# Performance work log

Hardware: AMD Instinct MI355X
Metric: run time of the kernel (lower is better)

## Reference

```python
import jax, jax.numpy as jnp
import numpy as np

VOCAB, EMB = 50000, 300
HID, FCH = 128, 64
B, T = 1024, 200


def setup_inputs() -> dict:
    key = jax.random.key(0)
    ks = jax.random.split(key, 10)
    s = 0.05
    return {
        "x": jax.random.randint(ks[0], (B, T), 0, VOCAB),
        "emb_table": jax.random.normal(ks[1], (VOCAB, EMB), jnp.float32) * s,
        "w_ih": jax.random.normal(ks[2], (4 * HID, EMB), jnp.float32) * s,
        "w_hh": jax.random.normal(ks[3], (4 * HID, HID), jnp.float32) * s,
        "b_ih": jax.random.normal(ks[4], (4 * HID,), jnp.float32) * s,
        "b_hh": jax.random.normal(ks[5], (4 * HID,), jnp.float32) * s,
        "fc1_w": jax.random.normal(ks[6], (FCH, HID), jnp.float32) * s,
        "fc1_b": jax.random.normal(ks[7], (FCH,), jnp.float32) * s,
        "fc2_w": jax.random.normal(ks[8], (1, FCH), jnp.float32) * s,
        "fc2_b": jax.random.normal(ks[9], (1,), jnp.float32) * s,
    }


def _lstm_last_h(e, w_ih, w_hh, b_ih, b_hh):
    # e: [B, T, E] -> final hidden state [B, H]
    b, t, _ = e.shape
    h_dim = w_hh.shape[1]
    # Precompute input projections for all timesteps: [T, B, 4H]
    xg = jnp.einsum('bte,ge->tbg', e, w_ih) + (b_ih + b_hh)

    def step(carry, xg_t):
        h, c = carry
        gates = xg_t + h @ w_hh.T  # [B, 4H]
        i, f, g, o = jnp.split(gates, 4, axis=-1)  # PyTorch gate order i,f,g,o
        i = jax.nn.sigmoid(i)
        f = jax.nn.sigmoid(f)
        g = jnp.tanh(g)
        o = jax.nn.sigmoid(o)
        c = f * c + i * g
        h = o * jnp.tanh(c)
        return (h, c), None

    h0 = jnp.zeros((b, h_dim), e.dtype)
    c0 = jnp.zeros((b, h_dim), e.dtype)
    (h_n, _), _ = jax.lax.scan(step, (h0, c0), xg)
    return h_n


def reference(x, emb_table, w_ih, w_hh, b_ih, b_hh, fc1_w, fc1_b, fc2_w, fc2_b):
    e = emb_table[x]  # [B, T, E]
    hn = _lstm_last_h(e, w_ih, w_hh, b_ih, b_hh)  # [B, H]
    # dropout is identity in eval mode
    h1 = jax.nn.relu(hn @ fc1_w.T + fc1_b)  # [B, FCH]
    logits = h1 @ fc2_w.T + fc2_b  # [B, 1]
    return jax.nn.sigmoid(logits)
```

## Files before the change

### kernel.cpp

```cpp
#include <hip/hip_runtime.h>
#include <hip/hip_bf16.h>
#include <stdint.h>

#define VOCAB 50000
#define EMB   300
#define EMBP  320
#define HID   128
#define NGATE 512
#define BATCH 1024
#define SEQ   200
#define ROWS  4
#define L2E   1.4426950408889634f

typedef __attribute__((ext_vector_type(8))) short short8;
typedef __attribute__((ext_vector_type(4))) float f32x4;

#define AS1 __attribute__((address_space(1)))
#define AS3 __attribute__((address_space(3)))

static __device__ __forceinline__ void gload_lds16(const void* g, void* s) {
  __builtin_amdgcn_global_load_lds((const AS1 uint32_t*)g, (AS3 uint32_t*)s, 16, 0, 0);
}

static __device__ __forceinline__ unsigned short f2bf(float f) {
  union { float f; unsigned u; } v; v.f = f;
  unsigned r = v.u + 0x7fffu + ((v.u >> 16) & 1u);
  return (unsigned short)(r >> 16);
}
static __device__ __forceinline__ float blo2f(unsigned u) {
  union { unsigned u; float f; } v; v.u = u << 16; return v.f;
}
static __device__ __forceinline__ float bhi2f(unsigned u) {
  union { unsigned u; float f; } v; v.u = u & 0xffff0000u; return v.f;
}
static __device__ __forceinline__ float sigmf(float x) {
  return __fdividef(1.0f, 1.0f + __expf(-x));
}
static __device__ __forceinline__ float sig2(float z) {
  return __builtin_amdgcn_rcpf(1.0f + __builtin_amdgcn_exp2f(-z));
}

__global__ void k_cvt_pad(const float* __restrict__ src, unsigned short* __restrict__ dst,
                          int rows, int sc, int dc, int perm, int smode) {
  int idx = blockIdx.x * blockDim.x + threadIdx.x;
  int cpr = dc >> 3;
  if (idx >= rows * cpr) return;
  int row = idx / cpr, k0 = (idx - row * cpr) * 8;
  float s = 1.0f;
  if (smode) s = ((row >> 7) == 2) ? (2.0f * L2E) : L2E;
  uint4 pack;
  unsigned short* v = (unsigned short*)&pack;
#pragma unroll
  for (int j = 0; j < 8; j++) {
    int k = k0 + j;
    v[j] = (k < sc) ? f2bf(src[(long)row * sc + k] * s) : (unsigned short)0;
  }
  int drow = perm ? ((row & 127) * 4 + (row >> 7)) : row;
  *(uint4*)(dst + (long)drow * dc + k0) = pack;
}

__global__ void k_bias(const float* __restrict__ a, const float* __restrict__ b,
                       float* __restrict__ o) {
  int i = blockIdx.x * blockDim.x + threadIdx.x;
  if (i < NGATE) {
    int g = i >> 7, hid = i & 127;
    float s = (g == 2) ? (2.0f * L2E) : L2E;
    o[hid * 4 + g] = (a[i] + b[i]) * s;
  }
}

__global__ __launch_bounds__(512, 4) void k_xg_gemm(
    const int* __restrict__ x, const unsigned short* __restrict__ embb,
    const unsigned short* __restrict__ wihb, const float* __restrict__ biasp,
    unsigned short* __restrict__ xg) {
  __shared__ __align__(16) unsigned short Al[2][128 * 64];
  __shared__ __align__(16) unsigned short Bl[2][128 * 64];
  const int tid = threadIdx.x;
  const int lane = tid & 63;
  const int bid = blockIdx.x;
  const int xcd = bid & 7;
  const int q = bid >> 3;
  const int tile_m = xcd * 200 + (q >> 2);
  const int tile_n = q & 3;
  const int t_idx = tile_m >> 3;
  const int b0 = (tile_m & 7) * 128;
  const int n0 = tile_n * 128;

  const int r0 = tid >> 3;
  const int sg = (tid & 7) ^ (r0 & 7);
  const unsigned short* asrc[2];
  const unsigned short* bsrc[2];
#pragma unroll
  for (int i = 0; i < 2; i++) {
    const int r = r0 + i * 64;
    const long ridx = x[(b0 + r) * SEQ + t_idx];
    asrc[i] = embb + ridx * EMBP + sg * 8;
    bsrc[i] = wihb + (long)(n0 + r) * EMBP + sg * 8;
  }

  const int wid = tid >> 6;
  const int wrow = wid >> 1, wcol = wid & 1;
  const int l15 = lane & 15, lgrp = lane >> 4;
  const int swz = (l15 & 7) << 4;

  f32x4 acc[2][4];
#pragma unroll
  for (int mt = 0; mt < 2; mt++)
#pragma unroll
    for (int nt = 0; nt < 4; nt++) acc[mt][nt] = (f32x4){0.f, 0.f, 0.f, 0.f};

#define STAGE(KS, BUF)                                                         \
  {                                                                            \
    _Pragma("unroll") for (int i = 0; i < 2; i++) {                            \
      gload_lds16(asrc[i] + (KS) * 64, (char*)Al + (BUF) * 16384 + tid * 16 + i * 8192); \
      gload_lds16(bsrc[i] + (KS) * 64, (char*)Bl + (BUF) * 16384 + tid * 16 + i * 8192); \
    }                                                                          \
  }

#define COMPUTE(BUF)                                                           \
  {                                                                            \
    const char* Ar = (const char*)Al + (BUF) * 16384 + (wrow * 32) * 128;      \
    const char* Br = (const char*)Bl + (BUF) * 16384 + (wcol * 64) * 128;      \
    _Pragma("unroll") for (int kt = 0; kt < 2; kt++) {                         \
      short8 af[2], bf[4];                                                     \
      _Pragma("unroll") for (int mt = 0; mt < 2; mt++)                         \
        af[mt] = *(const short8*)(Ar + (mt * 16 + l15) * 128 + ((kt * 64 + lgrp * 16) ^ swz)); \
      _Pragma("unroll") for (int nt = 0; nt < 4; nt++)                         \
        bf[nt] = *(const short8*)(Br + (nt * 16 + l15) * 128 + ((kt * 64 + lgrp * 16) ^ swz)); \
      _Pragma("unroll") for (int mt = 0; mt < 2; mt++)                         \
        _Pragma("unroll") for (int nt = 0; nt < 4; nt++)                       \
          acc[mt][nt] = __builtin_amdgcn_mfma_f32_16x16x32_bf16(af[mt], bf[nt], acc[mt][nt], 0, 0, 0); \
    }                                                                          \
  }

  STAGE(0, 0);
  __syncthreads();
  STAGE(1, 1); COMPUTE(0); __syncthreads();
  STAGE(2, 0); COMPUTE(1); __syncthreads();
  STAGE(3, 1); COMPUTE(0); __syncthreads();
  STAGE(4, 0); COMPUTE(1); __syncthreads();
  COMPUTE(0);
#undef STAGE
#undef COMPUTE

  const int m_base = tile_m * 128 + wrow * 32;
  const int colg = n0 + wcol * 64 + l15;
  const int rsub = lgrp * 4;
  float bv[4];
#pragma unroll
  for (int nt = 0; nt < 4; nt++) bv[nt] = biasp[colg + nt * 16];
#pragma unroll
  for (int mt = 0; mt < 2; mt++)
#pragma unroll
    for (int nt = 0; nt < 4; nt++)
#pragma unroll
      for (int j = 0; j < 4; j++) {
        const long m = m_base + mt * 16 + rsub + j;
        xg[m * NGATE + colg + nt * 16] = f2bf(acc[mt][nt][j] + bv[nt]);
      }
}

__global__ __launch_bounds__(512, 2) void k_lstm(
    const unsigned short* __restrict__ xg, const unsigned short* __restrict__ whhp,
    float* __restrict__ hfin) {
  __shared__ __align__(16) unsigned short h_lds[2 * 4 * 128];
  __shared__ __align__(16) float scratch[8 * 256];
  const int tid = threadIdx.x;
  const int lane = tid & 63;
  const int wid = tid >> 6;
  const int b0 = blockIdx.x * ROWS;
  const int l15 = lane & 15;
  const int lgrp = lane >> 4;
  const int hid = wid * 16 + l15;

  short8 wfr[4][4];
#pragma unroll
  for (int nt = 0; nt < 4; nt++)
#pragma unroll
    for (int kt = 0; kt < 4; kt++)
      wfr[nt][kt] = *(const short8*)(whhp + (long)(wid * 64 + nt * 16 + l15) * HID + kt * 32 + lgrp * 8);

  float c_r = 0.0f, h_r = 0.0f;

  ((unsigned*)h_lds)[tid] = 0;
  __syncthreads();

  const int ar = l15 & 3;
  int rdoff[4];
#pragma unroll
  for (int kt = 0; kt < 4; kt++)
    rdoff[kt] = ar * 256 + ((kt * 64 + lgrp * 16) ^ (ar << 5));
  const int hwoff = lgrp * 256 + ((2 * hid) ^ (lgrp << 5));
  const char* lb = (const char*)h_lds;

  float* sw = scratch + wid * 256;
  int swr[4];
#pragma unroll
  for (int nt = 0; nt < 4; nt++)
    swr[nt] = l15 * 64 + (((nt * 4 + lgrp) * 4) ^ (l15 * 4));
  const int srd = lgrp * 64 + ((l15 * 4) ^ (lgrp * 4));

  const unsigned short* xbase = xg + ((long)(b0 + lgrp) * HID + hid) * 4;
  const long TSTEP = (long)BATCH * HID * 4;
  uint2 xA = *(const uint2*)xbase;
  uint2 xB = *(const uint2*)(xbase + TSTEP);
  const unsigned short* xnext = xbase + 2 * TSTEP;

#define STEP_BODY(XS, RB, WB, T)                                               \
  {                                                                            \
    const float xf0 = blo2f(XS.x), xf1 = bhi2f(XS.x);                          \
    const float xf2 = blo2f(XS.y), xf3 = bhi2f(XS.y);                          \
    if ((T) + 2 < SEQ) XS = *(const uint2*)xnext;                              \
    short8 hf[4];                                                              \
    _Pragma("unroll") for (int kt = 0; kt < 4; kt++)                           \
      hf[kt] = *(const short8*)(lb + (RB) + rdoff[kt]);                        \
    f32x4 acc[4];                                                              \
    _Pragma("unroll") for (int nt = 0; nt < 4; nt++)                           \
      acc[nt] = (f32x4){0.f, 0.f, 0.f, 0.f};                                   \
    _Pragma("unroll") for (int kt = 0; kt < 4; kt++)                           \
      _Pragma("unroll") for (int nt = 0; nt < 4; nt++)                         \
        acc[nt] = __builtin_amdgcn_mfma_f32_16x16x32_bf16(wfr[nt][kt], hf[kt], \
                                                          acc[nt], 0, 0, 0);   \
    if (l15 < 4) {                                                             \
      _Pragma("unroll") for (int nt = 0; nt < 4; nt++)                         \
        *(f32x4*)(sw + swr[nt]) = acc[nt];                                     \
    }                                                                          \
    __builtin_amdgcn_sched_barrier(0);                                         \
    const f32x4 g4 = *(const f32x4*)(sw + srd);                                \
    const float zi = g4[0] + xf0;                                              \
    const float zf = g4[1] + xf1;                                              \
    const float zg = g4[2] + xf2;                                              \
    const float zo = g4[3] + xf3;                                              \
    const float iv = sig2(zi);                                                 \
    const float fv = sig2(zf);                                                 \
    const float gv = 2.0f * sig2(zg) - 1.0f;                                   \
    const float ov = sig2(zo);                                                 \
    c_r = fv * c_r + iv * gv;                                                  \
    const float tc = 2.0f * sig2(c_r * (2.0f * L2E)) - 1.0f;                   \
    h_r = ov * tc;                                                             \
    *(unsigned short*)((char*)h_lds + (WB) + hwoff) = f2bf(h_r);               \
    asm volatile("s_waitcnt lgkmcnt(0)" ::: "memory");                         \
    __builtin_amdgcn_s_barrier();                                              \
    __builtin_amdgcn_sched_barrier(0);                                         \
  }

  for (int t = 0; t < SEQ; t += 2) {
    STEP_BODY(xA, 0, 1024, t);
    xnext += TSTEP;
    STEP_BODY(xB, 1024, 0, t + 1);
    xnext += TSTEP;
  }
#undef STEP_BODY

  hfin[(b0 + lgrp) * HID + hid] = h_r;
}

__global__ void k_head(const float* __restrict__ hfin,
                       const float* __restrict__ fc1w, const float* __restrict__ fc1b,
                       const float* __restrict__ fc2w, const float* __restrict__ fc2b,
                       float* __restrict__ out) {
  const int tid = threadIdx.x;
  const int lane = tid & 63;
  const int wid = tid >> 6;
  const int row = blockIdx.x * 4 + wid;
  const float* h = hfin + row * HID;
  const float* w = fc1w + lane * HID;
  float acc = 0.0f;
#pragma unroll
  for (int k = 0; k < HID; k += 4) {
    const f32x4 hv = *(const f32x4*)(h + k);
    const f32x4 wv = *(const f32x4*)(w + k);
    acc += hv[0] * wv[0] + hv[1] * wv[1] + hv[2] * wv[2] + hv[3] * wv[3];
  }
  const float h1 = fmaxf(acc + fc1b[lane], 0.0f);
  float v = h1 * fc2w[lane];
#pragma unroll
  for (int off = 32; off > 0; off >>= 1) v += __shfl_down(v, off, 64);
  if (lane == 0) out[row] = sigmf(v + fc2b[0]);
}

extern "C" void kernel_launch(void* const* d_in, const int* in_sizes, int n_in,
                              void* d_out, int out_size, void* d_ws, size_t ws_size,
                              hipStream_t stream) {
  const int*   x    = (const int*)d_in[0];
  const float* emb  = (const float*)d_in[1];
  const float* w_ih = (const float*)d_in[2];
  const float* w_hh = (const float*)d_in[3];
  const float* b_ih = (const float*)d_in[4];
  const float* b_hh = (const float*)d_in[5];
  const float* fc1w = (const float*)d_in[6];
  const float* fc1b = (const float*)d_in[7];
  const float* fc2w = (const float*)d_in[8];
  const float* fc2b = (const float*)d_in[9];
  float* out = (float*)d_out;
  char* ws = (char*)d_ws;

  unsigned short* embb = (unsigned short*)(ws + 0);
  unsigned short* wihb = (unsigned short*)(ws + 32000000);
  unsigned short* whhp = (unsigned short*)(ws + 32327680);
  float*          biasp= (float*)(ws + 32458752);
  float*          hfinp= (float*)(ws + 32460800);
  unsigned short* xgb  = (unsigned short*)(ws + 32985088);

  k_cvt_pad<<<dim3((VOCAB * (EMBP / 8) + 255) / 256), dim3(256), 0, stream>>>(emb, embb, VOCAB, EMB, EMBP, 0, 0);
  k_cvt_pad<<<dim3((NGATE * (EMBP / 8) + 255) / 256), dim3(256), 0, stream>>>(w_ih, wihb, NGATE, EMB, EMBP, 1, 1);
  k_cvt_pad<<<dim3((NGATE * (HID / 8) + 255) / 256), dim3(256), 0, stream>>>(w_hh, whhp, NGATE, HID, HID, 1, 1);
  k_bias<<<dim3(2), dim3(256), 0, stream>>>(b_ih, b_hh, biasp);
  k_xg_gemm<<<dim3(1600 * 4), dim3(512), 0, stream>>>(x, embb, wihb, biasp, xgb);
  k_lstm<<<dim3(BATCH / ROWS), dim3(512), 0, stream>>>(xgb, whhp, hfinp);
  k_head<<<dim3(256), dim3(256), 0, stream>>>(hfinp, fc1w, fc1b, fc2w, fc2b, out);
  (void)in_sizes; (void)n_in; (void)out_size; (void)ws_size;
}
```

Before: 282.9 us.

## Fuse input-projection GEMM and LSTM recurrence with per-timestep completion flags

Merges the xg GEMM and the LSTM recurrence into one persistent launch. The first 256 blocks run the recurrence and spin on per-timestep atomic counters, while the remaining blocks compute GEMM tiles ordered by timestep and increment the counter for their step when done. The aim is to overlap the recurrence with the projection GEMM instead of running them back to back. The risks are spin-wait overhead, deadlock if the GEMM blocks cannot be scheduled while the LSTM blocks occupy the CUs, reduced occupancy from the shared 64KB LDS footprint, and use of the output buffer as flag storage before the head overwrites it.

```diff
diff --git a/kernel.cpp b/kernel.cpp
--- a/kernel.cpp
+++ b/kernel.cpp
@@ -60,54 +60,60 @@
 }
 
 __global__ void k_bias(const float* __restrict__ a, const float* __restrict__ b,
-                       float* __restrict__ o) {
+                       float* __restrict__ o, int* __restrict__ flags) {
   int i = blockIdx.x * blockDim.x + threadIdx.x;
   if (i < NGATE) {
     int g = i >> 7, hid = i & 127;
     float s = (g == 2) ? (2.0f * L2E) : L2E;
     o[hid * 4 + g] = (a[i] + b[i]) * s;
   }
-}
-
-__global__ __launch_bounds__(512, 4) void k_xg_gemm(
+  if (i < SEQ) flags[i] = 0;
+}
+
+__global__ __launch_bounds__(512, 4) void k_fused(
     const int* __restrict__ x, const unsigned short* __restrict__ embb,
     const unsigned short* __restrict__ wihb, const float* __restrict__ biasp,
-    unsigned short* __restrict__ xg) {
-  __shared__ __align__(16) unsigned short Al[2][128 * 64];
-  __shared__ __align__(16) unsigned short Bl[2][128 * 64];
+    unsigned short* __restrict__ xg, const unsigned short* __restrict__ whhp,
+    float* __restrict__ hfin, int* __restrict__ flags) {
+  __shared__ __align__(16) char smem[65536];
+  const int bid = blockIdx.x;
   const int tid = threadIdx.x;
   const int lane = tid & 63;
-  const int bid = blockIdx.x;
-  const int xcd = bid & 7;
-  const int q = bid >> 3;
-  const int tile_m = xcd * 200 + (q >> 2);
-  const int tile_n = q & 3;
-  const int t_idx = tile_m >> 3;
-  const int b0 = (tile_m & 7) * 128;
-  const int n0 = tile_n * 128;
-
-  const int r0 = tid >> 3;
-  const int sg = (tid & 7) ^ (r0 & 7);
-  const unsigned short* asrc[2];
-  const unsigned short* bsrc[2];
-#pragma unroll
-  for (int i = 0; i < 2; i++) {
-    const int r = r0 + i * 64;
-    const long ridx = x[(b0 + r) * SEQ + t_idx];
-    asrc[i] = embb + ridx * EMBP + sg * 8;
-    bsrc[i] = wihb + (long)(n0 + r) * EMBP + sg * 8;
-  }
-
-  const int wid = tid >> 6;
-  const int wrow = wid >> 1, wcol = wid & 1;
-  const int l15 = lane & 15, lgrp = lane >> 4;
-  const int swz = (l15 & 7) << 4;
-
-  f32x4 acc[2][4];
-#pragma unroll
-  for (int mt = 0; mt < 2; mt++)
-#pragma unroll
-    for (int nt = 0; nt < 4; nt++) acc[mt][nt] = (f32x4){0.f, 0.f, 0.f, 0.f};
+
+  if (bid >= 256) {
+    const int g = bid - 256;
+    const int t_ = g >> 5;
+    const int nb = (g >> 3) & 3;
+    const int mb = g & 7;
+    const int tile_m = t_ * 8 + mb;
+    const int t_idx = t_;
+    const int b0 = mb * 128;
+    const int n0 = nb * 128;
+    unsigned short* Al = (unsigned short*)smem;
+    unsigned short* Bl = (unsigned short*)(smem + 32768);
+
+    const int r0 = tid >> 3;
+    const int sg = (tid & 7) ^ (r0 & 7);
+    const unsigned short* asrc[2];
+    const unsigned short* bsrc[2];
+#pragma unroll
+    for (int i = 0; i < 2; i++) {
+      const int r = r0 + i * 64;
+      const long ridx = x[(b0 + r) * SEQ + t_idx];
+      asrc[i] = embb + ridx * EMBP + sg * 8;
+      bsrc[i] = wihb + (long)(n0 + r) * EMBP + sg * 8;
+    }
+
+    const int wid = tid >> 6;
+    const int wrow = wid >> 1, wcol = wid & 1;
+    const int l15 = lane & 15, lgrp = lane >> 4;
+    const int swz = (l15 & 7) << 4;
+
+    f32x4 acc[2][4];
+#pragma unroll
+    for (int mt = 0; mt < 2; mt++)
+#pragma unroll
+      for (int nt = 0; nt < 4; nt++) acc[mt][nt] = (f32x4){0.f, 0.f, 0.f, 0.f};
 
 #define STAGE(KS, BUF)                                                         \
   {                                                                            \
@@ -133,42 +139,42 @@
     }                                                                          \
   }
 
-  STAGE(0, 0);
-  __syncthreads();
-  STAGE(1, 1); COMPUTE(0); __syncthreads();
-  STAGE(2, 0); COMPUTE(1); __syncthreads();
-  STAGE(3, 1); COMPUTE(0); __syncthreads();
-  STAGE(4, 0); COMPUTE(1); __syncthreads();
-  COMPUTE(0);
+    STAGE(0, 0);
+    __syncthreads();
+    STAGE(1, 1); COMPUTE(0); __syncthreads();
+    STAGE(2, 0); COMPUTE(1); __syncthreads();
+    STAGE(3, 1); COMPUTE(0); __syncthreads();
+    STAGE(4, 0); COMPUTE(1); __syncthreads();
+    COMPUTE(0);
 #undef STAGE
 #undef COMPUTE
 
-  const int m_base = tile_m * 128 + wrow * 32;
-  const int colg = n0 + wcol * 64 + l15;
-  const int rsub = lgrp * 4;
-  float bv[4];
-#pragma unroll
-  for (int nt = 0; nt < 4; nt++) bv[nt] = biasp[colg + nt * 16];
-#pragma unroll
-  for (int mt = 0; mt < 2; mt++)
-#pragma unroll
-    for (int nt = 0; nt < 4; nt++)
-#pragma unroll
-      for (int j = 0; j < 4; j++) {
-        const long m = m_base + mt * 16 + rsub + j;
-        xg[m * NGATE + colg + nt * 16] = f2bf(acc[mt][nt][j] + bv[nt]);
-      }
-}
-
-__global__ __launch_bounds__(512, 2) void k_lstm(
-    const unsigned short* __restrict__ xg, const unsigned short* __restrict__ whhp,
-    float* __restrict__ hfin) {
-  __shared__ __align__(16) unsigned short h_lds[2 * 4 * 128];
-  __shared__ __align__(16) float scratch[8 * 256];
-  const int tid = threadIdx.x;
-  const int lane = tid & 63;
+    const int m_base = tile_m * 128 + wrow * 32;
+    const int colg = n0 + wcol * 64 + l15;
+    const int rsub = lgrp * 4;
+    float bv[4];
+#pragma unroll
+    for (int nt = 0; nt < 4; nt++) bv[nt] = biasp[colg + nt * 16];
+#pragma unroll
+    for (int mt = 0; mt < 2; mt++)
+#pragma unroll
+      for (int nt = 0; nt < 4; nt++)
+#pragma unroll
+        for (int j = 0; j < 4; j++) {
+          const long m = m_base + mt * 16 + rsub + j;
+          xg[m * NGATE + colg + nt * 16] = f2bf(acc[mt][nt][j] + bv[nt]);
+        }
+
+    __syncthreads();
+    if (tid == 0)
+      __hip_atomic_fetch_add(flags + t_, 1, __ATOMIC_RELEASE, __HIP_MEMORY_SCOPE_AGENT);
+    return;
+  }
+
+  unsigned short* h_lds = (unsigned short*)smem;
+  float* scratch = (float*)(smem + 2048);
   const int wid = tid >> 6;
-  const int b0 = blockIdx.x * ROWS;
+  const int b0 = bid * ROWS;
   const int l15 = lane & 15;
   const int lgrp = lane >> 4;
   const int hid = wid * 16 + l15;
@@ -202,15 +208,42 @@
 
   const unsigned short* xbase = xg + ((long)(b0 + lgrp) * HID + hid) * 4;
   const long TSTEP = (long)BATCH * HID * 4;
-  uint2 xA = *(const uint2*)xbase;
-  uint2 xB = *(const uint2*)(xbase + TSTEP);
+
+#define WAITF(T)                                                               \
+  {                                                                            \
+    int v = __hip_atomic_load(flags + (T), __ATOMIC_RELAXED, __HIP_MEMORY_SCOPE_AGENT); \
+    while (v < 32) {                                                           \
+      __builtin_amdgcn_s_sleep(2);                                             \
+      v = __hip_atomic_load(flags + (T), __ATOMIC_RELAXED, __HIP_MEMORY_SCOPE_AGENT); \
+    }                                                                          \
+  }
+#define XGLOAD(P)                                                              \
+  __builtin_bit_cast(uint2, __hip_atomic_load(                                 \
+      (const unsigned long long*)(P), __ATOMIC_RELAXED, __HIP_MEMORY_SCOPE_AGENT))
+
+  WAITF(0);
+  WAITF(1);
+  uint2 xA = XGLOAD(xbase);
+  uint2 xB = XGLOAD(xbase + TSTEP);
   const unsigned short* xnext = xbase + 2 * TSTEP;
+  int fv = __hip_atomic_load(flags + 2, __ATOMIC_RELAXED, __HIP_MEMORY_SCOPE_AGENT);
 
 #define STEP_BODY(XS, RB, WB, T)                                               \
   {                                                                            \
     const float xf0 = blo2f(XS.x), xf1 = bhi2f(XS.x);                          \
     const float xf2 = blo2f(XS.y), xf3 = bhi2f(XS.y);                          \
-    if ((T) + 2 < SEQ) XS = *(const uint2*)xnext;                              \
+    if ((T) + 2 < SEQ) {                                                       \
+      while (fv < 32) {                                                        \
+        __builtin_amdgcn_s_sleep(2);                                           \
+        fv = __hip_atomic_load(flags + (T) + 2, __ATOMIC_RELAXED,              \
+                               __HIP_MEMORY_SCOPE_AGENT);                      \
+      }                                                                        \
+      XS = XGLOAD(xnext);                                                      \
+      fv = ((T) + 3 < SEQ)                                                     \
+               ? __hip_atomic_load(flags + (T) + 3, __ATOMIC_RELAXED,          \
+                                   __HIP_MEMORY_SCOPE_AGENT)                   \
+               : 32;                                                           \
+    }                                                                          \
     short8 hf[4];                                                              \
     _Pragma("unroll") for (int kt = 0; kt < 4; kt++)                           \
       hf[kt] = *(const short8*)(lb + (RB) + rdoff[kt]);                        \
@@ -232,10 +265,10 @@
     const float zg = g4[2] + xf2;                                              \
     const float zo = g4[3] + xf3;                                              \
     const float iv = sig2(zi);                                                 \
-    const float fv = sig2(zf);                                                 \
+    const float fvv = sig2(zf);                                                \
     const float gv = 2.0f * sig2(zg) - 1.0f;                                   \
     const float ov = sig2(zo);                                                 \
-    c_r = fv * c_r + iv * gv;                                                  \
+    c_r = fvv * c_r + iv * gv;                                                 \
     const float tc = 2.0f * sig2(c_r * (2.0f * L2E)) - 1.0f;                   \
     h_r = ov * tc;                                                             \
     *(unsigned short*)((char*)h_lds + (WB) + hwoff) = f2bf(h_r);               \
@@ -251,6 +284,8 @@
     xnext += TSTEP;
   }
 #undef STEP_BODY
+#undef WAITF
+#undef XGLOAD
 
   hfin[(b0 + lgrp) * HID + hid] = h_r;
 }
@@ -301,13 +336,13 @@
   float*          biasp= (float*)(ws + 32458752);
   float*          hfinp= (float*)(ws + 32460800);
   unsigned short* xgb  = (unsigned short*)(ws + 32985088);
+  int* flags = (int*)d_out;
 
   k_cvt_pad<<<dim3((VOCAB * (EMBP / 8) + 255) / 256), dim3(256), 0, stream>>>(emb, embb, VOCAB, EMB, EMBP, 0, 0);
   k_cvt_pad<<<dim3((NGATE * (EMBP / 8) + 255) / 256), dim3(256), 0, stream>>>(w_ih, wihb, NGATE, EMB, EMBP, 1, 1);
   k_cvt_pad<<<dim3((NGATE * (HID / 8) + 255) / 256), dim3(256), 0, stream>>>(w_hh, whhp, NGATE, HID, HID, 1, 1);
-  k_bias<<<dim3(2), dim3(256), 0, stream>>>(b_ih, b_hh, biasp);
-  k_xg_gemm<<<dim3(1600 * 4), dim3(512), 0, stream>>>(x, embb, wihb, biasp, xgb);
-  k_lstm<<<dim3(BATCH / ROWS), dim3(512), 0, stream>>>(xgb, whhp, hfinp);
+  k_bias<<<dim3(2), dim3(256), 0, stream>>>(b_ih, b_hh, biasp, flags);
+  k_fused<<<dim3(256 + 1600 * 4), dim3(512), 0, stream>>>(x, embb, wihb, biasp, xgb, whhp, hfinp, flags);
   k_head<<<dim3(256), dim3(256), 0, stream>>>(hfinp, fc1w, fc1b, fc2w, fc2b, out);
   (void)in_sizes; (void)n_in; (void)out_size; (void)ws_size;
 }
```

Measured after the change: 965.2 us. 3.41x slower.
